# Performance work log

Hardware: AMD Instinct MI355X
Metric: run time of the kernel (lower is better)

The kernel has to match this reference:

```python
import jax, jax.numpy as jnp
import numpy as np

B, S, D = 2, 2048, 768
H, HD = 12, 64
ROT = 64            # head_dim * rope_dim_scale, even
LOCAL_WINDOW = 128
GLOBAL_EVERY = 3
GLOBAL_THETA = 160000.0
LOCAL_THETA = 10000.0


def setup_inputs() -> dict:
    key = jax.random.key(0)
    ks = jax.random.split(key, 5)
    sc = 1.0 / np.sqrt(D)
    return {
        "x": jax.random.normal(ks[0], (B, S, D), dtype=jnp.float32),
        "Wqkv": jax.random.normal(ks[1], (D, 3 * D), dtype=jnp.float32) * sc,
        "bqkv": jax.random.normal(ks[2], (3 * D,), dtype=jnp.float32) * 0.02,
        "Wout": jax.random.normal(ks[3], (D, D), dtype=jnp.float32) * sc,
        "bout": jax.random.normal(ks[4], (D,), dtype=jnp.float32) * 0.02,
        "layer_idx": 1,
    }


def _rope(q, k, seq_len, base):
    # q,k: [B,S,H,HD]; rotate first ROT dims with interleaved even/odd pairs
    dtype = q.dtype
    t = jnp.arange(seq_len, dtype=dtype)
    freqs = 1.0 / base ** (jnp.arange(0, ROT, 2, dtype=dtype) / ROT)  # [ROT/2]
    ang = t[:, None] * freqs[None, :]                                  # [S, ROT/2]
    cos = jnp.cos(ang)[None, :, None, :]
    sin = jnp.sin(ang)[None, :, None, :]

    def apply_rot(x):
        x1 = x[..., :ROT]
        even, odd = x1[..., ::2], x1[..., 1::2]
        re = even * cos - odd * sin
        ro = odd * cos + even * sin
        x1r = jnp.stack([re, ro], axis=-1).reshape(x1.shape)
        return jnp.concatenate([x1r, x[..., ROT:]], axis=-1)

    return apply_rot(q), apply_rot(k)


def reference(x, Wqkv, bqkv, Wout, bout, layer_idx):
    b, s, d = x.shape
    qkv = x @ Wqkv + bqkv                       # [B,S,3D]
    q, k, v = jnp.split(qkv, 3, axis=-1)
    q = q.reshape(b, s, H, HD)
    k = k.reshape(b, s, H, HD)
    v = v.reshape(b, s, H, HD)

    is_global = (layer_idx % GLOBAL_EVERY) == 0
    theta = GLOBAL_THETA if is_global else LOCAL_THETA
    q, k = _rope(q, k, s, theta)

    scores = jnp.einsum('bshd,bthd->bhst', q, k) / np.sqrt(HD)  # [B,H,S,S]
    if not is_global:
        idx = jnp.arange(s)
        mask = jnp.abs(idx[None, :] - idx[:, None]) > LOCAL_WINDOW  # [S,S]
        scores = jnp.where(mask[None, None], -jnp.inf, scores)

    attn = jax.nn.softmax(scores, axis=-1)
    out = jnp.einsum('bhst,bthd->bshd', attn, v).reshape(b, s, d)
    return out @ Wout + bout
```

## Files before the change

### kernel.cpp

```cpp
#include <hip/hip_runtime.h>
#include <hip/hip_bf16.h>
#include <math.h>

#define NB 2
#define NS 2048
#define ND 768
#define NH 12
#define HD 64
#define WIN 128
#define N_QKV 2304
#define QKN (NB * NH * NS * HD)

typedef __attribute__((ext_vector_type(8))) short short8;
typedef __attribute__((ext_vector_type(4))) short short4v;
typedef __attribute__((ext_vector_type(4))) float float4v;

static __device__ __forceinline__ short f2bf(float f) {
  __hip_bfloat16 h = __float2bfloat16(f);
  short s;
  __builtin_memcpy(&s, &h, 2);
  return s;
}

static __device__ __forceinline__ void async_copy16(void* lds, const void* g) {
  __builtin_amdgcn_global_load_lds(
      (const __attribute__((address_space(1))) unsigned int*)g,
      (__attribute__((address_space(3))) unsigned int*)(unsigned int)(unsigned long long)lds,
      16, 0, 0);
}

__global__ __launch_bounds__(256) void prep_kernel(
    const float* __restrict__ x, const float* __restrict__ Wqkv,
    const float* __restrict__ Wout, short* __restrict__ xb,
    short* __restrict__ Wqkvt, short* __restrict__ Woutt)
{
  __shared__ float t[32][33];
  const int u = blockIdx.x;
  const int tid = threadIdx.x;

  if (u < 3072) {
    const int i = u * 1024 + tid * 4;
    const float4 v = *(const float4*)(x + i);
    short4v o;
    o[0] = f2bf(v.x); o[1] = f2bf(v.y); o[2] = f2bf(v.z); o[3] = f2bf(v.w);
    *(short4v*)(xb + i) = o;
    return;
  }

  const bool isqkv = (u < 4800);
  const float* in = isqkv ? Wqkv : Wout;
  short* out = isqkv ? Wqkvt : Woutt;
  const int C = isqkv ? N_QKV : ND;
  const int tt = u - (isqkv ? 3072 : 4800);
  const int nbx = C / 32;
  const int bx = (tt % nbx) * 32;
  const int by = (tt / nbx) * 32;
  const int tx = tid & 31, ty = tid >> 5;
#pragma unroll
  for (int i = 0; i < 32; i += 8)
    t[ty + i][tx] = in[(size_t)(by + ty + i) * C + bx + tx];
  __syncthreads();
#pragma unroll
  for (int i = 0; i < 32; i += 8)
    out[(size_t)(bx + ty + i) * ND + by + tx] = f2bf(t[tx][ty + i]);
}

template <int MODE>
__global__ __launch_bounds__(256) void mfma_gemm128_kernel(
    const short* __restrict__ A, const short* __restrict__ Bt,
    const float* __restrict__ bias, const int* __restrict__ layer_idx_p,
    short* __restrict__ Qb, short* __restrict__ Kb, short* __restrict__ VT,
    float* __restrict__ Out, int K, int Ncols, int nTN, int mPerXcd)
{
  __shared__ short As[128 * 64];
  __shared__ short Bs[64 * 64];
  const int tid = threadIdx.x;
  const int w = tid >> 6, lane = tid & 63;
  const int c = lane & 15, g = lane >> 4;

  const int id = blockIdx.x;
  const int xcd = id & 7;
  const int k = id >> 3;
  const int mt = xcd * mPerXcd + k / nTN;
  const int nt = k - (k / nTN) * nTN;
  const int bm = mt * 128, bn = nt * 64;

  const int lr = lane >> 3;
  const int gch = (lane & 7) ^ lr;

  float4v acc[2][4];
#pragma unroll
  for (int i = 0; i < 2; ++i)
#pragma unroll
    for (int j = 0; j < 4; ++j) acc[i][j] = (float4v){0.f, 0.f, 0.f, 0.f};

  const short* Ag = A + (size_t)(bm + w * 32 + lr) * K + gch * 8;
  const short* Bg = Bt + (size_t)(bn + w * 16 + lr) * K + gch * 8;
  short* AsW = As + (w * 32) * 64;
  short* BsW = Bs + (w * 16) * 64;

  const int cl7 = c & 7;
  const short* aw = As + (w * 32 + c) * 64;
  const short* bwp = Bs + c * 64;

  for (int k0 = 0; k0 < K; k0 += 64) {
    async_copy16(AsW,        Ag + k0);
    async_copy16(AsW + 512,  Ag + k0 + (size_t)8 * K);
    async_copy16(AsW + 1024, Ag + k0 + (size_t)16 * K);
    async_copy16(AsW + 1536, Ag + k0 + (size_t)24 * K);
    async_copy16(BsW,        Bg + k0);
    async_copy16(BsW + 512,  Bg + k0 + (size_t)8 * K);
    __syncthreads();

    short8 af[2][2], bfr[4][2];
#pragma unroll
    for (int t = 0; t < 2; ++t) {
      const int slot = ((t * 4 + g) ^ cl7) * 8;
#pragma unroll
      for (int i = 0; i < 2; ++i) af[i][t] = *(const short8*)(aw + i * 16 * 64 + slot);
#pragma unroll
      for (int j = 0; j < 4; ++j) bfr[j][t] = *(const short8*)(bwp + j * 16 * 64 + slot);
    }
#pragma unroll
    for (int t = 0; t < 2; ++t)
#pragma unroll
      for (int i = 0; i < 2; ++i)
#pragma unroll
        for (int j = 0; j < 4; ++j)
          acc[i][j] = __builtin_amdgcn_mfma_f32_16x16x32_bf16(af[i][t], bfr[j][t], acc[i][j], 0, 0, 0);
    __syncthreads();
  }

  const int wm = bm + w * 32;
  const int wn = bn;
  float bj[4];
#pragma unroll
  for (int j = 0; j < 4; ++j) bj[j] = bias[wn + j * 16 + c];

  if (MODE == 1) {
#pragma unroll
    for (int i = 0; i < 2; ++i)
#pragma unroll
      for (int j = 0; j < 4; ++j)
#pragma unroll
        for (int r = 0; r < 4; ++r)
          Out[(size_t)(wm + i * 16 + 4 * g + r) * Ncols + wn + j * 16 + c] =
              acc[i][j][r] + bj[j];
  } else {
    const int which = bn / ND;
    const int hd0 = wn - which * ND;
    const int h = hd0 >> 6;
    const int bidx = bm >> 11;
    const int srow = (bm & (NS - 1)) + w * 32;

    if (which == 2) {
#pragma unroll
      for (int j = 0; j < 4; ++j) {
        const int d = j * 16 + c;
        short* vbase = VT + ((size_t)(bidx * NH + h) * HD + d) * NS;
#pragma unroll
        for (int i = 0; i < 2; ++i) {
          short4v v4;
#pragma unroll
          for (int r = 0; r < 4; ++r) v4[r] = f2bf(acc[i][j][r] + bj[j]);
          *(short4v*)(vbase + srow + i * 16 + 4 * g) = v4;
        }
      }
    } else {
      const bool is_global = ((*layer_idx_p) % 3) == 0;
      const float theta = is_global ? 160000.0f : 10000.0f;
      const float nlt = -__logf(theta) * (1.0f / 64.0f);
      short* dst = which ? Kb : Qb;
      const bool oddc = (c & 1);
#pragma unroll
      for (int j = 0; j < 4; ++j) {
        const int d = j * 16 + c;
        const float freq = __expf((float)(d & ~1) * nlt);
#pragma unroll
        for (int i = 0; i < 2; ++i) {
#pragma unroll
          for (int r = 0; r < 4; ++r) {
            const float val = acc[i][j][r] + bj[j];
            const float partner = __shfl_xor(val, 1);
            const int s = srow + i * 16 + 4 * g + r;
            float sn, cs;
            __sincosf((float)s * freq, &sn, &cs);
            const float o = oddc ? (val * cs + partner * sn)
                                 : (val * cs - partner * sn);
            dst[((size_t)(bidx * NH + h) * NS + s) * HD + d] = f2bf(o);
          }
        }
      }
    }
  }
}

__global__ __launch_bounds__(256) void attn_mfma_kernel(
    const short* __restrict__ Qb, const short* __restrict__ Kb,
    const short* __restrict__ VT, short* __restrict__ CTXb,
    const int* __restrict__ layer_idx_p)
{
  const int lane = threadIdx.x & 63;
  const int wv = threadIdx.x >> 6;
  const int c = lane & 15;
  const int g = lane >> 4;

  const int id = blockIdx.x;
  const int xcd = id & 7;
  const int k = id >> 3;
  const int bh = xcd * 3 + (k >> 5);
  const int qt = k & 31;

  const int b = bh / NH;
  const int h = bh - b * NH;
  const int q0 = qt * 64 + wv * 16;
  const bool is_global = ((*layer_idx_p) % 3) == 0;
  const size_t base = (size_t)bh * NS * HD;

  const short* qrow = Qb + base + (size_t)(q0 + c) * HD + g * 8;
  const short8 qf0 = *(const short8*)(qrow);
  const short8 qf1 = *(const short8*)(qrow + 32);

  float4v O0 = {0.f, 0.f, 0.f, 0.f}, O1 = O0, O2 = O0, O3 = O0;
  float lacc = 0.0f;
  const int q = q0 + c;

  const int lo = is_global ? 0 : q0 - 128;
  const int hi = is_global ? (NS - 1) : q0 + 143;

  for (int kt = lo; kt <= hi; kt += 32) {
    if (kt + 31 < 0 || kt >= NS) continue;

    const int k1c = min(max(kt + c, 0), NS - 1);
    const int k2c = min(max(kt + 16 + c, 0), NS - 1);
    const short* kr1 = Kb + base + (size_t)k1c * HD + g * 8;
    const short* kr2 = Kb + base + (size_t)k2c * HD + g * 8;
    const short8 kf10 = *(const short8*)kr1;
    const short8 kf11 = *(const short8*)(kr1 + 32);
    const short8 kf20 = *(const short8*)kr2;
    const short8 kf21 = *(const short8*)(kr2 + 32);
    float4v st1 = {0.f, 0.f, 0.f, 0.f}, st2 = {0.f, 0.f, 0.f, 0.f};
    st1 = __builtin_amdgcn_mfma_f32_16x16x32_bf16(kf10, qf0, st1, 0, 0, 0);
    st1 = __builtin_amdgcn_mfma_f32_16x16x32_bf16(kf11, qf1, st1, 0, 0, 0);
    st2 = __builtin_amdgcn_mfma_f32_16x16x32_bf16(kf20, qf0, st2, 0, 0, 0);
    st2 = __builtin_amdgcn_mfma_f32_16x16x32_bf16(kf21, qf1, st2, 0, 0, 0);

    float p1[4], p2[4];
#pragma unroll
    for (int r = 0; r < 4; ++r) {
      const int key1 = kt + 4 * g + r;
      const int key2 = key1 + 16;
      const bool v1 = (key1 >= 0) & (key1 < NS) &
                      (is_global | ((key1 - q <= WIN) & (q - key1 <= WIN)));
      const bool v2 = (key2 >= 0) & (key2 < NS) &
                      (is_global | ((key2 - q <= WIN) & (q - key2 <= WIN)));
      p1[r] = __expf(v1 ? st1[r] * 0.125f : -1e30f);
      p2[r] = __expf(v2 ? st2[r] * 0.125f : -1e30f);
      lacc += p1[r] + p2[r];
    }

    const int srcA = (2 * (g & 1)) * 16 + c;
    const int srcB = srcA + 16;
    short8 pf;
#pragma unroll
    for (int r = 0; r < 4; ++r) {
      const float f1a = __shfl(p1[r], srcA);
      const float f1b = __shfl(p1[r], srcB);
      const float f2a = __shfl(p2[r], srcA);
      const float f2b = __shfl(p2[r], srcB);
      pf[r]     = f2bf((g < 2) ? f1a : f2a);
      pf[4 + r] = f2bf((g < 2) ? f1b : f2b);
    }

    const int ks = min(max(kt + 8 * g, 0), NS - 8);
    const short* vrow = VT + base + (size_t)c * NS + ks;
    const short8 vf0 = *(const short8*)(vrow);
    const short8 vf1 = *(const short8*)(vrow + 16 * NS);
    const short8 vf2 = *(const short8*)(vrow + 32 * NS);
    const short8 vf3 = *(const short8*)(vrow + 48 * NS);
    O0 = __builtin_amdgcn_mfma_f32_16x16x32_bf16(vf0, pf, O0, 0, 0, 0);
    O1 = __builtin_amdgcn_mfma_f32_16x16x32_bf16(vf1, pf, O1, 0, 0, 0);
    O2 = __builtin_amdgcn_mfma_f32_16x16x32_bf16(vf2, pf, O2, 0, 0, 0);
    O3 = __builtin_amdgcn_mfma_f32_16x16x32_bf16(vf3, pf, O3, 0, 0, 0);
  }

  lacc += __shfl_xor(lacc, 16);
  lacc += __shfl_xor(lacc, 32);
  const float inv = 1.0f / lacc;
  short* crow = CTXb + ((size_t)(b * NS + q) * NH + h) * HD;
#pragma unroll
  for (int r = 0; r < 4; ++r) {
    const int d = 4 * g + r;
    crow[d]      = f2bf(O0[r] * inv);
    crow[d + 16] = f2bf(O1[r] * inv);
    crow[d + 32] = f2bf(O2[r] * inv);
    crow[d + 48] = f2bf(O3[r] * inv);
  }
}

extern "C" void kernel_launch(void* const* d_in, const int* in_sizes, int n_in,
                              void* d_out, int out_size, void* d_ws, size_t ws_size,
                              hipStream_t stream) {
  const float* x    = (const float*)d_in[0];
  const float* Wqkv = (const float*)d_in[1];
  const float* bqkv = (const float*)d_in[2];
  const float* Wout = (const float*)d_in[3];
  const float* bout = (const float*)d_in[4];
  const int* layer_idx = (const int*)d_in[5];

  short* xb    = (short*)d_ws;
  short* Wqkvt = xb + (size_t)NB * NS * ND;
  short* Woutt = Wqkvt + (size_t)ND * N_QKV;
  short* Qb    = Woutt + (size_t)ND * ND;
  short* Kb    = Qb + (size_t)QKN;
  short* VT    = Kb + (size_t)QKN;
  short* CTXb  = VT + (size_t)QKN;

  prep_kernel<<<5376, 256, 0, stream>>>(x, Wqkv, Wout, xb, Wqkvt, Woutt);

  mfma_gemm128_kernel<0><<<1152, 256, 0, stream>>>(
      xb, Wqkvt, bqkv, layer_idx, Qb, Kb, VT, nullptr, ND, N_QKV, 36, 4);

  attn_mfma_kernel<<<NB * NH * (NS / 64), 256, 0, stream>>>(Qb, Kb, VT, CTXb, layer_idx);

  mfma_gemm128_kernel<1><<<384, 256, 0, stream>>>(
      CTXb, Woutt, bout, layer_idx, nullptr, nullptr, nullptr, (float*)d_out, ND, ND, 12, 4);
}
```

Baseline: 146.6 us.

## Split attention key range across two wave groups with LDS reduction

Doubles the attention block to 512 threads. Two groups of four waves each process half of the key tiles for the same 16-query rows: the local window is split 5/4 and the global range is split in halves. Each wave writes its partial output accumulators and softmax denominator to shared memory, and the first group adds the second group's partials before normalizing and storing. The aim is to shorten each wave's serial loop over key tiles and raise parallelism. In exchange it adds about 35 KB of LDS per block, a block-wide barrier, and reduction traffic.

```diff
diff --git a/kernel.cpp b/kernel.cpp
--- a/kernel.cpp
+++ b/kernel.cpp
@@ -195,13 +195,17 @@
   }
 }
 
-__global__ __launch_bounds__(256) void attn_mfma_kernel(
+__global__ __launch_bounds__(512) void attn_mfma_kernel(
     const short* __restrict__ Qb, const short* __restrict__ Kb,
     const short* __restrict__ VT, short* __restrict__ CTXb,
     const int* __restrict__ layer_idx_p)
 {
-  const int lane = threadIdx.x & 63;
-  const int wv = threadIdx.x >> 6;
+  __shared__ float red[8][17][64];
+  const int tid = threadIdx.x;
+  const int lane = tid & 63;
+  const int wv = tid >> 6;
+  const int half = wv >> 2;
+  const int wq = wv & 3;
   const int c = lane & 15;
   const int g = lane >> 4;
 
@@ -213,7 +217,7 @@
 
   const int b = bh / NH;
   const int h = bh - b * NH;
-  const int q0 = qt * 64 + wv * 16;
+  const int q0 = qt * 64 + wq * 16;
   const bool is_global = ((*layer_idx_p) % 3) == 0;
   const size_t base = (size_t)bh * NS * HD;
 
@@ -225,8 +229,14 @@
   float lacc = 0.0f;
   const int q = q0 + c;
 
-  const int lo = is_global ? 0 : q0 - 128;
-  const int hi = is_global ? (NS - 1) : q0 + 143;
+  int lo, hi;
+  if (!is_global) {
+    lo = half ? (q0 + 32)  : (q0 - 128);
+    hi = half ? (q0 + 128) : (q0);
+  } else {
+    lo = half ? (NS / 2)      : 0;
+    hi = half ? (NS - 32)     : (NS / 2 - 32);
+  }
 
   for (int kt = lo; kt <= hi; kt += 32) {
     if (kt + 31 < 0 || kt >= NS) continue;
@@ -284,6 +294,27 @@
     O3 = __builtin_amdgcn_mfma_f32_16x16x32_bf16(vf3, pf, O3, 0, 0, 0);
   }
 
+  red[wv][16][lane] = lacc;
+#pragma unroll
+  for (int r = 0; r < 4; ++r) {
+    red[wv][r][lane]      = O0[r];
+    red[wv][4 + r][lane]  = O1[r];
+    red[wv][8 + r][lane]  = O2[r];
+    red[wv][12 + r][lane] = O3[r];
+  }
+  __syncthreads();
+  if (half) return;
+
+  const float* pr = &red[wv + 4][0][lane];
+#pragma unroll
+  for (int r = 0; r < 4; ++r) {
+    O0[r] += pr[(r)      * 64];
+    O1[r] += pr[(4 + r)  * 64];
+    O2[r] += pr[(8 + r)  * 64];
+    O3[r] += pr[(12 + r) * 64];
+  }
+  lacc += pr[16 * 64];
+
   lacc += __shfl_xor(lacc, 16);
   lacc += __shfl_xor(lacc, 32);
   const float inv = 1.0f / lacc;
@@ -321,7 +352,7 @@
   mfma_gemm128_kernel<0><<<1152, 256, 0, stream>>>(
       xb, Wqkvt, bqkv, layer_idx, Qb, Kb, VT, nullptr, ND, N_QKV, 36, 4);
 
-  attn_mfma_kernel<<<NB * NH * (NS / 64), 256, 0, stream>>>(Qb, Kb, VT, CTXb, layer_idx);
+  attn_mfma_kernel<<<NB * NH * (NS / 64), 512, 0, stream>>>(Qb, Kb, VT, CTXb, layer_idx);
 
   mfma_gemm128_kernel<1><<<384, 256, 0, stream>>>(
       CTXb, Woutt, bout, layer_idx, nullptr, nullptr, nullptr, (float*)d_out, ND, ND, 12, 4);
```

Measured after the change: 147.9 us. About the same (+0.9%).
